# Kernel optimization log

Hardware: AMD Instinct MI355X
Metric: run time of the kernel (lower is better)

## Reference

```python
import jax, jax.numpy as jnp
import numpy as np

N_NODES = 200000
D_IN = 256
D_OUT = 256
B = 4096
K1 = 25   # layer-1 fanout
K2 = 10   # layer-2 fanout
M = B * (1 + K2)  # layer-1 node set size: batch centers + their sampled neighbors


def setup_inputs() -> dict:
    key = jax.random.key(0)
    k1, k2, k3, k4, k5, k6 = jax.random.split(key, 6)
    features = jax.random.normal(k1, (N_NODES, D_IN), dtype=jnp.float32)
    # SageLayer weights: [out, 2*in] (concat path, gcn=False); small kaiming-like scale
    W1 = jax.random.normal(k2, (D_OUT, 2 * D_IN), dtype=jnp.float32) * 0.05
    W2 = jax.random.normal(k3, (D_OUT, 2 * D_OUT), dtype=jnp.float32) * 0.05
    nodes_batch = jax.random.randint(k4, (B,), 0, N_NODES, dtype=jnp.int64)
    neigh2 = jax.random.randint(k5, (B, K2), 0, N_NODES, dtype=jnp.int64)
    neigh1 = jax.random.randint(k6, (M, K1), 0, N_NODES, dtype=jnp.int64)
    return {"features": features, "W1": W1, "W2": W2,
            "nodes_batch": nodes_batch, "neigh2": neigh2, "neigh1": neigh1}


def reference(features, W1, W2, nodes_batch, neigh2, neigh1):
    # Layer-1 node set: centers first, then their sampled layer-2 neighbors.
    l1_nodes = jnp.concatenate([nodes_batch, neigh2.reshape(-1)])  # [M]
    # ---- layer 1: MEAN aggregate over K1 sampled neighbors (gather + mean) ----
    agg1 = jnp.mean(features[neigh1], axis=1)          # [M, K1, D_IN] -> [M, D_IN]
    self1 = features[l1_nodes]                         # [M, D_IN]
    # SageLayer: relu(W.mm(cat(self, agg).T)).T == relu(cat @ W.T)
    h1 = jax.nn.relu(jnp.concatenate([self1, agg1], axis=1) @ W1.T)  # [M, D_OUT]
    # ---- layer 2: centers are h1[:B]; neighbor embeddings are h1[B:] in blocks of K2 ----
    nb = nodes_batch.shape[0]
    agg2 = jnp.mean(h1[nb:].reshape(nb, -1, h1.shape[1]), axis=1)    # [B, D_OUT]
    h2 = jax.nn.relu(jnp.concatenate([h1[:nb], agg2], axis=1) @ W2.T)  # [B, D_OUT]
    return h2
```

## Files before the change

kernel.cpp:

```cpp
#include <hip/hip_runtime.h>
#include <hip/hip_bf16.h>

typedef __attribute__((ext_vector_type(8))) short bf16x8;
typedef __attribute__((ext_vector_type(4))) float f32x4;
typedef __attribute__((ext_vector_type(2))) float f32x2;

#define B_SZ   4096
#define K1     25
#define K2     10
#define M_L1   45056
#define D      256
#define K_DIM  512
#define N_NODES 200000

static __device__ __forceinline__ unsigned short f2bf(float f) {
    union { float f; unsigned u; } v; v.f = f;
    return (unsigned short)((v.u + 0x7fffu + ((v.u >> 16) & 1u)) >> 16);
}
static __device__ __forceinline__ float bf2f(unsigned short h) {
    union { unsigned u; float f; } v; v.u = ((unsigned)h) << 16;
    return v.f;
}

__global__ __launch_bounds__(256)
void convert_fp8(const float* __restrict__ f, unsigned* __restrict__ f8) {
    const size_t i = ((size_t)blockIdx.x * 256 + threadIdx.x) * 8;
    const float4 a = *(const float4*)(f + i);
    const float4 b = *(const float4*)(f + i + 4);
    unsigned u0 = 0, u1 = 0;
    u0 = __builtin_amdgcn_cvt_pk_fp8_f32(a.x, a.y, u0, false);
    u0 = __builtin_amdgcn_cvt_pk_fp8_f32(a.z, a.w, u0, true);
    u1 = __builtin_amdgcn_cvt_pk_fp8_f32(b.x, b.y, u1, false);
    u1 = __builtin_amdgcn_cvt_pk_fp8_f32(b.z, b.w, u1, true);
    uint2 r; r.x = u0; r.y = u1;
    *(uint2*)(f8 + (i >> 2)) = r;
}

__global__ __launch_bounds__(256)
void convert_w(const float* __restrict__ W1, const float* __restrict__ W2,
               unsigned short* __restrict__ W1b, unsigned short* __restrict__ W2b) {
    const int i = blockIdx.x * 256 + threadIdx.x;
    W1b[i] = f2bf(W1[i]);
    W2b[i] = f2bf(W2[i]);
}

__global__ __launch_bounds__(256)
void agg1_kernel(const float* __restrict__ feat,
                 const unsigned* __restrict__ f8,
                 const int* __restrict__ nodes_batch,
                 const int* __restrict__ neigh2,
                 const int* __restrict__ neigh1,
                 unsigned short* __restrict__ X1) {
    const int wave = threadIdx.x >> 6;
    const int lane = threadIdx.x & 63;
    const int m = (blockIdx.x << 2) + wave;
    const int self_node = (m < B_SZ) ? nodes_batch[m] : neigh2[m - B_SZ];
    const int* nb = neigh1 + (size_t)m * K1;

    int idxv = (lane < K1) ? nb[lane] : 0;
    const float4 s = *(const float4*)(feat + (size_t)self_node * D + (lane << 2));

    unsigned q[K1];
    #pragma unroll
    for (int j = 0; j < K1; ++j) {
        const int node = __shfl(idxv, j);
        q[j] = f8[(size_t)node * (D / 4) + lane];
    }

    float a0 = 0.f, a1 = 0.f, a2 = 0.f, a3 = 0.f;
    #pragma unroll
    for (int j = 0; j < K1; ++j) {
        const f32x2 lo = __builtin_amdgcn_cvt_pk_f32_fp8(q[j], false);
        const f32x2 hi = __builtin_amdgcn_cvt_pk_f32_fp8(q[j], true);
        a0 += lo.x; a1 += lo.y; a2 += hi.x; a3 += hi.y;
    }
    const float inv = 1.0f / (float)K1;

    unsigned short* xr = X1 + (size_t)m * K_DIM;
    *(ushort4*)(xr + (lane << 2)) =
        make_ushort4(f2bf(s.x), f2bf(s.y), f2bf(s.z), f2bf(s.w));
    *(ushort4*)(xr + D + (lane << 2)) =
        make_ushort4(f2bf(a0 * inv), f2bf(a1 * inv), f2bf(a2 * inv), f2bf(a3 * inv));
}

__global__ __launch_bounds__(256)
void agg2_kernel(const unsigned short* __restrict__ h1,
                 unsigned short* __restrict__ X2) {
    const int wave = threadIdx.x >> 6;
    const int lane = threadIdx.x & 63;
    const int b = (blockIdx.x << 2) + wave;
    const ushort4 s = *(const ushort4*)(h1 + (size_t)b * D + (lane << 2));
    float sx = 0.f, sy = 0.f, sz = 0.f, sw = 0.f;
    #pragma unroll
    for (int k = 0; k < K2; ++k) {
        const ushort4 v = *(const ushort4*)(h1 + (size_t)(B_SZ + b * K2 + k) * D + (lane << 2));
        sx += bf2f(v.x); sy += bf2f(v.y); sz += bf2f(v.z); sw += bf2f(v.w);
    }
    const float inv = 1.0f / (float)K2;
    unsigned short* xr = X2 + (size_t)b * K_DIM;
    *(ushort4*)(xr + (lane << 2)) = s;
    *(ushort4*)(xr + D + (lane << 2)) =
        make_ushort4(f2bf(sx * inv), f2bf(sy * inv), f2bf(sz * inv), f2bf(sw * inv));
}

template<bool OUT_BF16>
__global__ __launch_bounds__(256)
void gemm_relu(const unsigned short* __restrict__ A,
               const unsigned short* __restrict__ W,
               void* __restrict__ Cout) {
    __shared__ unsigned short As[128 * 64];
    __shared__ unsigned short Bs[128 * 64];
    const int tid  = threadIdx.x;
    const int w    = tid >> 6, lane = tid & 63;
    const int quad = lane >> 4, l16 = lane & 15;
    const int wm = (w >> 1) << 6;
    const int wn = (w & 1) << 6;
    const size_t row0 = (size_t)blockIdx.x * 128;
    const size_t col0 = (size_t)blockIdx.y * 128;

    const int srow   = (w << 5) + (lane >> 3);
    const int schunk = ((lane & 7) ^ (lane >> 3)) << 3;
    const unsigned short* aG = A + (row0 + srow) * K_DIM + schunk;
    const unsigned short* bG = W + (col0 + srow) * K_DIM + schunk;

    f32x4 acc[4][4];
    #pragma unroll
    for (int i = 0; i < 4; ++i)
        #pragma unroll
        for (int j = 0; j < 4; ++j)
            acc[i][j] = (f32x4){0.f, 0.f, 0.f, 0.f};

    for (int k0 = 0; k0 < K_DIM; k0 += 64) {
        __syncthreads();
        #pragma unroll
        for (int n = 0; n < 4; ++n) {
            __builtin_amdgcn_global_load_lds(
                (const __attribute__((address_space(1))) void*)(aG + (size_t)(n * 8) * K_DIM + k0),
                (__attribute__((address_space(3))) void*)(As + ((w << 2) + n) * 512),
                16, 0, 0);
            __builtin_amdgcn_global_load_lds(
                (const __attribute__((address_space(1))) void*)(bG + (size_t)(n * 8) * K_DIM + k0),
                (__attribute__((address_space(3))) void*)(Bs + ((w << 2) + n) * 512),
                16, 0, 0);
        }
        __syncthreads();
        #pragma unroll
        for (int ks = 0; ks < 2; ++ks) {
            bf16x8 af[4], bfr[4];
            #pragma unroll
            for (int i = 0; i < 4; ++i) {
                const int row = wm + i * 16 + l16;
                af[i] = *(const bf16x8*)&As[row * 64 + ((((ks << 2) + quad) ^ (l16 & 7)) << 3)];
            }
            #pragma unroll
            for (int i = 0; i < 4; ++i) {
                const int row = wn + i * 16 + l16;
                bfr[i] = *(const bf16x8*)&Bs[row * 64 + ((((ks << 2) + quad) ^ (l16 & 7)) << 3)];
            }
            #pragma unroll
            for (int mi = 0; mi < 4; ++mi)
                #pragma unroll
                for (int ni = 0; ni < 4; ++ni)
                    acc[mi][ni] = __builtin_amdgcn_mfma_f32_16x16x32_bf16(
                        af[mi], bfr[ni], acc[mi][ni], 0, 0, 0);
        }
    }

    #pragma unroll
    for (int mi = 0; mi < 4; ++mi) {
        #pragma unroll
        for (int ni = 0; ni < 4; ++ni) {
            #pragma unroll
            for (int r = 0; r < 4; ++r) {
                const size_t gm = row0 + wm + mi * 16 + quad * 4 + r;
                const size_t gn = col0 + wn + ni * 16 + l16;
                float v = acc[mi][ni][r];
                v = v > 0.f ? v : 0.f;
                if (OUT_BF16)
                    ((unsigned short*)Cout)[gm * D + gn] = f2bf(v);
                else
                    ((float*)Cout)[gm * D + gn] = v;
            }
        }
    }
}

extern "C" void kernel_launch(void* const* d_in, const int* in_sizes, int n_in,
                              void* d_out, int out_size, void* d_ws, size_t ws_size,
                              hipStream_t stream) {
    const float* feat        = (const float*)d_in[0];
    const float* W1          = (const float*)d_in[1];
    const float* W2          = (const float*)d_in[2];
    const int*   nodes_batch = (const int*)d_in[3];
    const int*   neigh2      = (const int*)d_in[4];
    const int*   neigh1      = (const int*)d_in[5];
    float* out = (float*)d_out;

    char* ws = (char*)d_ws;
    unsigned*       f8   = (unsigned*)(ws);
    unsigned short* X1   = (unsigned short*)(ws + 51200000);
    unsigned short* h1   = (unsigned short*)(ws + 51200000 + 46137344);
    unsigned short* X2   = (unsigned short*)(ws + 51200000 + 46137344 + 23068672);
    unsigned short* W1b  = (unsigned short*)(ws + 51200000 + 46137344 + 23068672 + 4194304);
    unsigned short* W2b  = (unsigned short*)(ws + 51200000 + 46137344 + 23068672 + 4194304 + 262144);

    convert_fp8<<<25000, 256, 0, stream>>>(feat, f8);
    convert_w<<<512, 256, 0, stream>>>(W1, W2, W1b, W2b);
    agg1_kernel<<<M_L1 / 4, 256, 0, stream>>>(feat, f8, nodes_batch, neigh2, neigh1, X1);
    gemm_relu<true><<<dim3(M_L1 / 128, 2), 256, 0, stream>>>(X1, W1b, h1);
    agg2_kernel<<<B_SZ / 4, 256, 0, stream>>>(h1, X2);
    gemm_relu<false><<<dim3(B_SZ / 128, 2), 256, 0, stream>>>(X2, W2b, out);
}
```

Baseline: 378.5 us.

## Fuse layer-1 gather-aggregate with GEMM via shared-memory tile

Replaces the separate layer-1 aggregation kernel and GEMM with one kernel. Each block gathers and averages 64 rows into a swizzled LDS tile and multiplies it against W1 read directly from global memory, then writes h1. This removes the round trip of the X1 intermediate through HBM and one launch. In exchange it uses 64KB of LDS per block, which lowers occupancy, and reads W1 without LDS staging.

```diff
diff --git a/kernel.cpp b/kernel.cpp
--- a/kernel.cpp
+++ b/kernel.cpp
@@ -45,42 +45,91 @@
 }
 
 __global__ __launch_bounds__(256)
-void agg1_kernel(const float* __restrict__ feat,
-                 const unsigned* __restrict__ f8,
-                 const int* __restrict__ nodes_batch,
-                 const int* __restrict__ neigh2,
-                 const int* __restrict__ neigh1,
-                 unsigned short* __restrict__ X1) {
-    const int wave = threadIdx.x >> 6;
-    const int lane = threadIdx.x & 63;
-    const int m = (blockIdx.x << 2) + wave;
-    const int self_node = (m < B_SZ) ? nodes_batch[m] : neigh2[m - B_SZ];
-    const int* nb = neigh1 + (size_t)m * K1;
-
-    int idxv = (lane < K1) ? nb[lane] : 0;
-    const float4 s = *(const float4*)(feat + (size_t)self_node * D + (lane << 2));
-
-    unsigned q[K1];
-    #pragma unroll
-    for (int j = 0; j < K1; ++j) {
-        const int node = __shfl(idxv, j);
-        q[j] = f8[(size_t)node * (D / 4) + lane];
-    }
-
-    float a0 = 0.f, a1 = 0.f, a2 = 0.f, a3 = 0.f;
-    #pragma unroll
-    for (int j = 0; j < K1; ++j) {
-        const f32x2 lo = __builtin_amdgcn_cvt_pk_f32_fp8(q[j], false);
-        const f32x2 hi = __builtin_amdgcn_cvt_pk_f32_fp8(q[j], true);
-        a0 += lo.x; a1 += lo.y; a2 += hi.x; a3 += hi.y;
-    }
-    const float inv = 1.0f / (float)K1;
-
-    unsigned short* xr = X1 + (size_t)m * K_DIM;
-    *(ushort4*)(xr + (lane << 2)) =
-        make_ushort4(f2bf(s.x), f2bf(s.y), f2bf(s.z), f2bf(s.w));
-    *(ushort4*)(xr + D + (lane << 2)) =
-        make_ushort4(f2bf(a0 * inv), f2bf(a1 * inv), f2bf(a2 * inv), f2bf(a3 * inv));
+void fused_l1(const float* __restrict__ feat,
+              const unsigned* __restrict__ f8,
+              const int* __restrict__ nodes_batch,
+              const int* __restrict__ neigh2,
+              const int* __restrict__ neigh1,
+              const unsigned short* __restrict__ W1b,
+              unsigned short* __restrict__ h1) {
+    __shared__ unsigned short At[64 * 512];
+    const int tid  = threadIdx.x;
+    const int w    = tid >> 6, lane = tid & 63;
+    const int quad = lane >> 4, l16 = lane & 15;
+    const int row0 = blockIdx.x << 6;
+
+    for (int t = 0; t < 16; ++t) {
+        const int r = (w << 4) + t;
+        const int m = row0 + r;
+        const int self_node = (m < B_SZ) ? nodes_batch[m] : neigh2[m - B_SZ];
+        const int* nb = neigh1 + (size_t)m * K1;
+        int idxv = (lane < K1) ? nb[lane] : 0;
+        const float4 s = *(const float4*)(feat + (size_t)self_node * D + (lane << 2));
+        unsigned q[K1];
+        #pragma unroll
+        for (int j = 0; j < K1; ++j)
+            q[j] = f8[(size_t)__shfl(idxv, j) * (D / 4) + lane];
+        float a0 = 0.f, a1 = 0.f, a2 = 0.f, a3 = 0.f;
+        #pragma unroll
+        for (int j = 0; j < K1; ++j) {
+            const f32x2 lo = __builtin_amdgcn_cvt_pk_f32_fp8(q[j], false);
+            const f32x2 hi = __builtin_amdgcn_cvt_pk_f32_fp8(q[j], true);
+            a0 += lo.x; a1 += lo.y; a2 += hi.x; a3 += hi.y;
+        }
+        const float inv = 1.0f / (float)K1;
+        const int cs = lane >> 1;
+        const int ca = 32 + cs;
+        const int slotS = (cs & 56) | ((cs ^ r) & 7);
+        const int slotA = (ca & 56) | ((ca ^ r) & 7);
+        const int sub = (lane & 1) << 2;
+        *(ushort4*)&At[r * 512 + slotS * 8 + sub] =
+            make_ushort4(f2bf(s.x), f2bf(s.y), f2bf(s.z), f2bf(s.w));
+        *(ushort4*)&At[r * 512 + slotA * 8 + sub] =
+            make_ushort4(f2bf(a0 * inv), f2bf(a1 * inv), f2bf(a2 * inv), f2bf(a3 * inv));
+    }
+    __syncthreads();
+
+    const int wn = w << 6;
+    f32x4 acc[4][4];
+    #pragma unroll
+    for (int i = 0; i < 4; ++i)
+        #pragma unroll
+        for (int j = 0; j < 4; ++j)
+            acc[i][j] = (f32x4){0.f, 0.f, 0.f, 0.f};
+
+    #pragma unroll 4
+    for (int s = 0; s < 16; ++s) {
+        bf16x8 bfr[4], af[4];
+        #pragma unroll
+        for (int ni = 0; ni < 4; ++ni)
+            bfr[ni] = *(const bf16x8*)(W1b +
+                (size_t)(wn + ni * 16 + l16) * K_DIM + s * 32 + quad * 8);
+        #pragma unroll
+        for (int mi = 0; mi < 4; ++mi) {
+            const int rr = mi * 16 + l16;
+            const int c = (s << 2) + quad;
+            const int slot = (c & 56) | ((c ^ rr) & 7);
+            af[mi] = *(const bf16x8*)&At[rr * 512 + slot * 8];
+        }
+        #pragma unroll
+        for (int mi = 0; mi < 4; ++mi)
+            #pragma unroll
+            for (int ni = 0; ni < 4; ++ni)
+                acc[mi][ni] = __builtin_amdgcn_mfma_f32_16x16x32_bf16(
+                    af[mi], bfr[ni], acc[mi][ni], 0, 0, 0);
+    }
+
+    #pragma unroll
+    for (int mi = 0; mi < 4; ++mi)
+        #pragma unroll
+        for (int ni = 0; ni < 4; ++ni)
+            #pragma unroll
+            for (int r = 0; r < 4; ++r) {
+                const size_t gm = (size_t)row0 + mi * 16 + quad * 4 + r;
+                const size_t gn = wn + ni * 16 + l16;
+                float v = acc[mi][ni][r];
+                h1[gm * D + gn] = f2bf(v > 0.f ? v : 0.f);
+            }
 }
 
 __global__ __launch_bounds__(256)
@@ -198,16 +247,14 @@
 
     char* ws = (char*)d_ws;
     unsigned*       f8   = (unsigned*)(ws);
-    unsigned short* X1   = (unsigned short*)(ws + 51200000);
-    unsigned short* h1   = (unsigned short*)(ws + 51200000 + 46137344);
-    unsigned short* X2   = (unsigned short*)(ws + 51200000 + 46137344 + 23068672);
-    unsigned short* W1b  = (unsigned short*)(ws + 51200000 + 46137344 + 23068672 + 4194304);
-    unsigned short* W2b  = (unsigned short*)(ws + 51200000 + 46137344 + 23068672 + 4194304 + 262144);
+    unsigned short* h1   = (unsigned short*)(ws + 51200000);
+    unsigned short* X2   = (unsigned short*)(ws + 51200000 + 23068672);
+    unsigned short* W1b  = (unsigned short*)(ws + 51200000 + 23068672 + 4194304);
+    unsigned short* W2b  = (unsigned short*)(ws + 51200000 + 23068672 + 4194304 + 262144);
 
     convert_fp8<<<25000, 256, 0, stream>>>(feat, f8);
     convert_w<<<512, 256, 0, stream>>>(W1, W2, W1b, W2b);
-    agg1_kernel<<<M_L1 / 4, 256, 0, stream>>>(feat, f8, nodes_batch, neigh2, neigh1, X1);
-    gemm_relu<true><<<dim3(M_L1 / 128, 2), 256, 0, stream>>>(X1, W1b, h1);
+    fused_l1<<<M_L1 / 64, 256, 0, stream>>>(feat, f8, nodes_batch, neigh2, neigh1, W1b, h1);
     agg2_kernel<<<B_SZ / 4, 256, 0, stream>>>(h1, X2);
     gemm_relu<false><<<dim3(B_SZ / 128, 2), 256, 0, stream>>>(X2, W2b, out);
 }
```

New measurement: 386.3 us. +2.1%, slower.
